# Performance work log

Measured on AMD Instinct MI355X. Metric: run time of the kernel, lower is better.

The kernel has to match this reference:

```python
import jax, jax.numpy as jnp
import numpy as np


def fps(pts, m):
    # pts: [N,3]; iterative farthest point sampling, deterministic start at index 0
    d0 = jnp.sum((pts - pts[0]) ** 2, axis=-1)  # [N]
    def step(mind, _):
        nxt = jnp.argmax(mind)
        d = jnp.sum((pts - pts[nxt]) ** 2, axis=-1)
        return jnp.minimum(mind, d), nxt
    _, idxs = jax.lax.scan(step, d0, None, length=m - 1)
    return jnp.concatenate([jnp.zeros((1,), idxs.dtype), idxs])  # [m]


def knn(queries, pts, k):
    # queries [M,3], pts [N,3] -> [M,k] indices of k nearest points (includes self)
    d = (jnp.sum(queries ** 2, -1, keepdims=True)
         - 2.0 * queries @ pts.T
         + jnp.sum(pts ** 2, -1)[None, :])  # [M,N]
    _, idx = jax.lax.top_k(-d, k)
    return idx


def mlp(x, params):
    # shared PointNet MLP: Linear+ReLU stack
    for w, b in params:
        x = jax.nn.relu(x @ w + b)
    return x


def sa_level(points, feats, ratio, k, params):
    # set-abstraction: fps downsample -> knn group -> shared MLP -> max pool per cluster
    B, N, _ = points.shape
    m = int(N * ratio)
    sel = jax.vmap(lambda p: fps(p, m))(points)                      # [B,m]
    npts = jnp.take_along_axis(points, sel[..., None], axis=1)       # [B,m,3]
    nbr = jax.vmap(knn, in_axes=(0, 0, None))(npts, points, k)       # [B,m,k]
    C = feats.shape[-1]
    kf = jnp.take_along_axis(feats, nbr.reshape(B, m * k, 1), axis=1).reshape(B, m, k, C)
    h = mlp(kf, params)                                              # [B,m,k,out]
    return npts, jnp.max(h, axis=2)                                  # [B,m,3], [B,m,out]


def setup_inputs() -> dict:
    key = jax.random.key(0)
    ks = jax.random.split(key, 20)
    points = jax.random.normal(ks[0], (8, 8192, 3), dtype=jnp.float32)
    batch = jnp.repeat(jnp.arange(8, dtype=jnp.int64), 8192)
    dims = {
        'pn1': [(3, 8), (8, 16), (16, 16)],
        'pn2': [(16, 32), (32, 64), (64, 64)],
        'pn3': [(64, 128), (128, 256), (256, 256)],
    }
    inp = {'points': points, 'batch': batch}
    i = 1
    for name, shapes in dims.items():
        for j, (cin, cout) in enumerate(shapes, start=1):
            inp[f'{name}_w{j}'] = jax.random.normal(ks[i], (cin, cout), dtype=jnp.float32) * (1.0 / np.sqrt(cin))
            inp[f'{name}_b{j}'] = jnp.zeros((cout,), dtype=jnp.float32)
            i += 1
    return inp


def reference(points, batch,
              pn1_w1, pn1_b1, pn1_w2, pn1_b2, pn1_w3, pn1_b3,
              pn2_w1, pn2_b1, pn2_w2, pn2_b2, pn2_w3, pn2_b3,
              pn3_w1, pn3_b1, pn3_w2, pn3_b2, pn3_w3, pn3_b3):
    # batch is implied by the uniform [B,N,3] layout (all clouds equal size)
    p1 = [(pn1_w1, pn1_b1), (pn1_w2, pn1_b2), (pn1_w3, pn1_b3)]
    p2 = [(pn2_w1, pn2_b1), (pn2_w2, pn2_b2), (pn2_w3, pn2_b3)]
    p3 = [(pn3_w1, pn3_b1), (pn3_w2, pn3_b2), (pn3_w3, pn3_b3)]
    pts1, f1 = sa_level(points, points, 0.25, 4, p1)   # [8,2048,3], [8,2048,16]
    pts2, f2 = sa_level(pts1, f1, 0.25, 4, p2)         # [8,512,3], [8,512,64]
    # level 3: cluster == batch -> global max pool per cloud
    out = jnp.max(mlp(f2, p3), axis=1)                  # [8,256]
    return out
```

## Files before the change

### kernel.cpp

```cpp
#include <hip/hip_runtime.h>
#include <stdint.h>

typedef unsigned long long u64;
typedef unsigned int u32;
typedef float f2 __attribute__((ext_vector_type(2)));

__device__ __forceinline__ float rn_mul(float a, float b){ return __fmul_rn(a,b); }
__device__ __forceinline__ float rn_add(float a, float b){ return __fadd_rn(a,b); }
__device__ __forceinline__ float rn_sub(float a, float b){ return __fsub_rn(a,b); }

__device__ __forceinline__ u32 fkey(float d){
  u32 b = __float_as_uint(d);
  return b ^ ((u32)((int)b >> 31) | 0x80000000u);
}

__device__ __forceinline__ u64 shfl_xor64(u64 v, int mask){
  int lo = __shfl_xor((int)(u32)v, mask, 64);
  int hi = __shfl_xor((int)(u32)(v >> 32), mask, 64);
  return ((u64)(u32)hi << 32) | (u32)lo;
}
__device__ __forceinline__ u64 umin64(u64 a, u64 b){ return a < b ? a : b; }
__device__ __forceinline__ u64 umax64(u64 a, u64 b){ return a > b ? a : b; }

template<int C>
__device__ __forceinline__ u64 dstep64(u64 v){
  const u32 l = (u32)__builtin_amdgcn_update_dpp((int)(u32)v, (int)(u32)v, C, 0xF, 0xF, false);
  const u32 h = (u32)__builtin_amdgcn_update_dpp((int)(u32)(v>>32), (int)(u32)(v>>32), C, 0xF, 0xF, false);
  const u64 o = ((u64)h << 32) | l;
  return o > v ? o : v;
}
__device__ __forceinline__ u64 wave64_max64(u64 v){
  v = dstep64<0x111>(v); v = dstep64<0x112>(v); v = dstep64<0x114>(v);
  v = dstep64<0x118>(v); v = dstep64<0x142>(v); v = dstep64<0x143>(v);
  return v;
}

template<int N, int NT, int M>
__global__ __launch_bounds__(NT)
void fps_kernel(const float* __restrict__ pts, float* __restrict__ npts)
{
#pragma clang fp contract(off)
  constexpr int PPT = N / NT;
  constexpr int PP2 = PPT / 2;
  constexpr int NW  = NT / 64;
  __shared__ float4 sp[N];
  __shared__ unsigned short WX[M];
  __shared__ u64 part[2][NW];
  const int b = blockIdx.x;
  const float* P = pts + (size_t)b * N * 3;
  float* O = npts + (size_t)b * M * 3;
  const int tid = threadIdx.x, lane = tid & 63, wv = tid >> 6;

  for (int i = tid; i < N; i += NT)
    sp[i] = make_float4(P[3*i+0], P[3*i+1], P[3*i+2], 0.0f);
  if (tid == 0) WX[0] = 0;
  __syncthreads();

  f2 rx[PP2], ry[PP2], rz[PP2], mind[PP2];
  const float4 c0 = sp[0];
  {
    const f2 cx2 = {c0.x,c0.x}, cy2 = {c0.y,c0.y}, cz2 = {c0.z,c0.z};
#pragma unroll
    for (int j = 0; j < PP2; ++j){
      const float4 va = sp[tid + (2*j+0)*NT];
      const float4 vb = sp[tid + (2*j+1)*NT];
      rx[j] = f2{va.x, vb.x}; ry[j] = f2{va.y, vb.y}; rz[j] = f2{va.z, vb.z};
      const f2 dx = rx[j]-cx2, dy = ry[j]-cy2, dz = rz[j]-cz2;
      mind[j] = ((dx*dx) + (dy*dy)) + (dz*dz);
    }
  }

#define LANEPK(dstpk)                                                         \
  {                                                                           \
    u64 p_[PPT];                                                              \
    _Pragma("unroll")                                                         \
    for (int k = 0; k < PPT; ++k){                                            \
      const float mk = (k&1) ? mind[k>>1].y : mind[k>>1].x;                   \
      p_[k] = ((u64)__float_as_uint(mk) << 32)                                \
            | (u64)(u32)~(u32)(tid + k*NT);                                   \
    }                                                                         \
    _Pragma("unroll")                                                         \
    for (int s = PPT/2; s > 0; s >>= 1)                                       \
      for (int i = 0; i < s; ++i) p_[i] = umax64(p_[i], p_[i+s]);             \
    (dstpk) = wave64_max64(p_[0]);                                            \
  }

  u64 mypk; LANEPK(mypk)

  for (int it = 1; it < M; ++it){
    if (lane == 63) part[it & 1][wv] = mypk;
    __syncthreads();
    u64 v = part[it & 1][lane & (NW-1)];
    v = dstep64<0x111>(v); v = dstep64<0x112>(v);
    const u32 wl = (u32)__builtin_amdgcn_readlane((int)(u32)v, 3);
    const u32 widx = ~wl;
    if (tid == 0) WX[it] = (unsigned short)widx;
    const float4 c = sp[widx];
    const f2 cx2 = {c.x,c.x}, cy2 = {c.y,c.y}, cz2 = {c.z,c.z};
#pragma unroll
    for (int j = 0; j < PP2; ++j){
      const f2 dx = rx[j]-cx2, dy = ry[j]-cy2, dz = rz[j]-cz2;
      const f2 d = ((dx*dx) + (dy*dy)) + (dz*dz);
      mind[j].x = fminf(mind[j].x, d.x);
      mind[j].y = fminf(mind[j].y, d.y);
    }
    LANEPK(mypk)
  }
  __syncthreads();
  for (int j = tid; j < M; j += NT){
    const float4 v = sp[WX[j]];
    O[3*j+0] = v.x; O[3*j+1] = v.y; O[3*j+2] = v.z;
  }
#undef LANEPK
}

__device__ __forceinline__ void top4_insert(u64& a0,u64& a1,u64& a2,u64& a3, u64 p){
  if (p < a3){
    const bool c2 = p < a2, c1 = p < a1, c0 = p < a0;
    const u64 n3 = c2 ? a2 : p;
    const u64 n2 = c2 ? (c1 ? a1 : p) : a2;
    const u64 n1 = c1 ? (c0 ? a0 : p) : a1;
    const u64 n0 = c0 ? p : a0;
    a0=n0; a1=n1; a2=n2; a3=n3;
  }
}

__device__ __forceinline__ void merge4_local(u64& a0,u64& a1,u64& a2,u64& a3,
                                             u64 b0,u64 b1,u64 b2,u64 b3){
  const u64 m0 = umin64(a0, b3);
  const u64 m1 = umin64(a1, b2);
  const u64 m2 = umin64(a2, b1);
  const u64 m3 = umin64(a3, b0);
  const u64 lo02 = umin64(m0,m2), hi02 = umax64(m0,m2);
  const u64 lo13 = umin64(m1,m3), hi13 = umax64(m1,m3);
  a0 = umin64(lo02, lo13); a1 = umax64(lo02, lo13);
  a2 = umin64(hi02, hi13); a3 = umax64(hi02, hi13);
}

__device__ __forceinline__ void merge4(u64& a0, u64& a1, u64& a2, u64& a3, int st)
{
  const u64 b0 = shfl_xor64(a0, st);
  const u64 b1 = shfl_xor64(a1, st);
  const u64 b2 = shfl_xor64(a2, st);
  const u64 b3 = shfl_xor64(a3, st);
  merge4_local(a0,a1,a2,a3, b0,b1,b2,b3);
}

template<int N, int M, int CH>
__global__ __launch_bounds__(256)
void knn_mlp1_kernel(const float* __restrict__ q, const float* __restrict__ pts,
                     const float* __restrict__ w1, const float* __restrict__ b1,
                     const float* __restrict__ w2, const float* __restrict__ b2,
                     const float* __restrict__ w3, const float* __restrict__ b3,
                     float* __restrict__ f1)
{
  __shared__ float4 s4[CH];
  constexpr int QPB = 64;
  const int blk = blockIdx.x;
  const int b = blk / (M / QPB);
  const int chunk = blk % (M / QPB);
  const int tid = threadIdx.x;
  const int g = tid >> 2;
  const int r = tid & 3;
  const int qi = chunk * QPB + g;
  const float* qp = q + ((size_t)b * M + qi) * 3;
  const float qx = qp[0], qy = qp[1], qz = qp[2];
  const float sumq = rn_add(rn_add(rn_mul(qx,qx), rn_mul(qy,qy)), rn_mul(qz,qz));
  const float* P = pts + (size_t)b * N * 3;

  u64 a0=~0ull, a1=~0ull, a2=~0ull, a3=~0ull;
  u64 e0=~0ull, e1=~0ull, e2=~0ull, e3=~0ull;
  for (int c0 = 0; c0 < N; c0 += CH){
    for (int i = tid; i < CH; i += 256){
      const float x = P[3*(c0+i)+0], y = P[3*(c0+i)+1], z = P[3*(c0+i)+2];
      s4[i] = make_float4(x, y, z,
          rn_add(rn_add(rn_mul(x,x), rn_mul(y,y)), rn_mul(z,z)));
    }
    __syncthreads();
#pragma unroll 2
    for (int jj = r; jj < CH; jj += 8){
      { const float4 v = s4[jj];
        const float dot = rn_add(rn_add(rn_mul(qx,v.x), rn_mul(qy,v.y)),
                                 rn_mul(qz,v.z));
        const float d = rn_add(rn_sub(sumq, rn_mul(2.0f, dot)), v.w);
        top4_insert(a0,a1,a2,a3, ((u64)fkey(d) << 32) | (u32)(c0+jj)); }
      { const float4 v = s4[jj+4];
        const float dot = rn_add(rn_add(rn_mul(qx,v.x), rn_mul(qy,v.y)),
                                 rn_mul(qz,v.z));
        const float d = rn_add(rn_sub(sumq, rn_mul(2.0f, dot)), v.w);
        top4_insert(e0,e1,e2,e3, ((u64)fkey(d) << 32) | (u32)(c0+jj+4)); }
    }
    __syncthreads();
  }
  merge4_local(a0,a1,a2,a3, e0,e1,e2,e3);
  merge4(a0,a1,a2,a3,1);
  merge4(a0,a1,a2,a3,2);
  const u64 selp = (r==0) ? a0 : (r==1) ? a1 : (r==2) ? a2 : a3;
  const u32 nidx = (u32)selp;

  const float nx = P[3*nidx+0], ny = P[3*nidx+1], nz = P[3*nidx+2];
  float h1[8];
#pragma unroll
  for (int c = 0; c < 8; ++c){
    float acc = b1[c];
    acc = fmaf(nx, w1[0*8+c], acc);
    acc = fmaf(ny, w1[1*8+c], acc);
    acc = fmaf(nz, w1[2*8+c], acc);
    h1[c] = fmaxf(acc, 0.0f);
  }
  float h2[16];
#pragma unroll
  for (int c = 0; c < 16; ++c){
    float acc = b2[c];
#pragma unroll
    for (int k = 0; k < 8; ++k) acc = fmaf(h1[k], w2[k*16+c], acc);
    h2[c] = fmaxf(acc, 0.0f);
  }
  float* fo = f1 + ((size_t)b * M + qi) * 16;
#pragma unroll
  for (int c = 0; c < 16; ++c){
    float acc = b3[c];
#pragma unroll
    for (int k = 0; k < 16; ++k) acc = fmaf(h2[k], w3[k*16+c], acc);
    float v = fmaxf(acc, 0.0f);
    v = fmaxf(v, __shfl_xor(v, 1, 64));
    v = fmaxf(v, __shfl_xor(v, 2, 64));
    if (r == 0) fo[c] = v;
  }
}

__global__ __launch_bounds__(256)
void knn_mlp2_kernel(const float* __restrict__ q, const float* __restrict__ pts,
                     const float* __restrict__ f1,
                     const float* __restrict__ w1, const float* __restrict__ b1,
                     const float* __restrict__ w2, const float* __restrict__ b2,
                     const float* __restrict__ w3, const float* __restrict__ b3,
                     float* __restrict__ f2)
{
  constexpr int N = 2048, M = 512, QPB = 64, QSTR = 2048;
  __shared__ float4 s4[N];
  const int blk = blockIdx.x;
  const int b = blk / (M / QPB);
  const int chunk = blk % (M / QPB);
  const int tid = threadIdx.x;
  const int g = tid >> 2;
  const int r = tid & 3;
  const int qi = chunk * QPB + g;
  const float* qp = q + ((size_t)b * QSTR + qi) * 3;
  const float qx = qp[0], qy = qp[1], qz = qp[2];
  const float sumq = rn_add(rn_add(rn_mul(qx,qx), rn_mul(qy,qy)), rn_mul(qz,qz));
  const float* P = pts + (size_t)b * N * 3;

  for (int i = tid; i < N; i += 256){
    const float x = P[3*i+0], y = P[3*i+1], z = P[3*i+2];
    s4[i] = make_float4(x, y, z,
        rn_add(rn_add(rn_mul(x,x), rn_mul(y,y)), rn_mul(z,z)));
  }
  __syncthreads();

  u64 a0=~0ull, a1=~0ull, a2=~0ull, a3=~0ull;
  u64 e0=~0ull, e1=~0ull, e2=~0ull, e3=~0ull;
#pragma unroll 2
  for (int j = r; j < N; j += 8){
    { const float4 v = s4[j];
      const float dot = rn_add(rn_add(rn_mul(qx,v.x), rn_mul(qy,v.y)),
                               rn_mul(qz,v.z));
      const float d = rn_add(rn_sub(sumq, rn_mul(2.0f, dot)), v.w);
      top4_insert(a0,a1,a2,a3, ((u64)fkey(d) << 32) | (u32)j); }
    { const float4 v = s4[j+4];
      const float dot = rn_add(rn_add(rn_mul(qx,v.x), rn_mul(qy,v.y)),
                               rn_mul(qz,v.z));
      const float d = rn_add(rn_sub(sumq, rn_mul(2.0f, dot)), v.w);
      top4_insert(e0,e1,e2,e3, ((u64)fkey(d) << 32) | (u32)(j+4)); }
  }
  merge4_local(a0,a1,a2,a3, e0,e1,e2,e3);
  merge4(a0,a1,a2,a3,1);
  merge4(a0,a1,a2,a3,2);
  const u64 selp = (r==0) ? a0 : (r==1) ? a1 : (r==2) ? a2 : a3;
  const u32 nidx = (u32)selp;

  const float* fv = f1 + ((size_t)b * 2048 + nidx) * 16;
  float x[16];
#pragma unroll
  for (int i = 0; i < 4; ++i){
    const float4 v = ((const float4*)fv)[i];
    x[4*i+0]=v.x; x[4*i+1]=v.y; x[4*i+2]=v.z; x[4*i+3]=v.w;
  }
  float h1[32];
#pragma unroll
  for (int c = 0; c < 32; ++c){
    float acc = b1[c];
#pragma unroll
    for (int k = 0; k < 16; ++k) acc = fmaf(x[k], w1[k*32+c], acc);
    h1[c] = fmaxf(acc, 0.0f);
  }
  float h2[64];
#pragma unroll
  for (int c = 0; c < 64; ++c){
    float acc = b2[c];
#pragma unroll
    for (int k = 0; k < 32; ++k) acc = fmaf(h1[k], w2[k*64+c], acc);
    h2[c] = fmaxf(acc, 0.0f);
  }
  float* fo = f2 + ((size_t)b * M + qi) * 64;
#pragma unroll
  for (int c = 0; c < 64; ++c){
    float acc = b3[c];
#pragma unroll
    for (int k = 0; k < 64; ++k) acc = fmaf(h2[k], w3[k*64+c], acc);
    float v = fmaxf(acc, 0.0f);
    v = fmaxf(v, __shfl_xor(v, 1, 64));
    v = fmaxf(v, __shfl_xor(v, 2, 64));
    if (r == 0) fo[c] = v;
  }
}

__global__ __launch_bounds__(256)
void mlp3_kernel(const float* __restrict__ f2,
                 const float* __restrict__ w1, const float* __restrict__ b1,
                 const float* __restrict__ w2, const float* __restrict__ b2,
                 const float* __restrict__ w3, const float* __restrict__ b3,
                 float* __restrict__ out)
{
  constexpr int P = 16;
  __shared__ float X [P][64];
  __shared__ float H1[P][128];
  __shared__ float H2[P][256];
  __shared__ float PM[4][256];
  const int blk = blockIdx.x;
  const int b  = blk >> 5;
  const int pc = blk & 31;
  const int tid = threadIdx.x;
  const float* F = f2 + ((size_t)b * 512 + (size_t)pc * P) * 64;
  { const float4 v = ((const float4*)F)[tid]; ((float4*)&X[0][0])[tid] = v; }
  __syncthreads();
  {
    const int p = tid >> 4, c0 = (tid & 15) * 8;
    float acc[8];
#pragma unroll
    for (int i = 0; i < 8; ++i) acc[i] = b1[c0+i];
    for (int k = 0; k < 64; ++k){
      const float xv = X[p][k];
      const float4 wa = *(const float4*)&w1[k*128 + c0];
      const float4 wb = *(const float4*)&w1[k*128 + c0 + 4];
      acc[0]=fmaf(xv,wa.x,acc[0]); acc[1]=fmaf(xv,wa.y,acc[1]);
      acc[2]=fmaf(xv,wa.z,acc[2]); acc[3]=fmaf(xv,wa.w,acc[3]);
      acc[4]=fmaf(xv,wb.x,acc[4]); acc[5]=fmaf(xv,wb.y,acc[5]);
      acc[6]=fmaf(xv,wb.z,acc[6]); acc[7]=fmaf(xv,wb.w,acc[7]);
    }
#pragma unroll
    for (int i = 0; i < 8; ++i) H1[p][c0+i] = fmaxf(acc[i], 0.0f);
  }
  __syncthreads();
  {
    const int p = tid >> 4, c0 = (tid & 15) * 16;
    float acc[16];
#pragma unroll
    for (int i = 0; i < 16; ++i) acc[i] = b2[c0+i];
    for (int k = 0; k < 128; ++k){
      const float xv = H1[p][k];
#pragma unroll
      for (int i4 = 0; i4 < 4; ++i4){
        const float4 wv = *(const float4*)&w2[k*256 + c0 + 4*i4];
        acc[4*i4+0]=fmaf(xv,wv.x,acc[4*i4+0]);
        acc[4*i4+1]=fmaf(xv,wv.y,acc[4*i4+1]);
        acc[4*i4+2]=fmaf(xv,wv.z,acc[4*i4+2]);
        acc[4*i4+3]=fmaf(xv,wv.w,acc[4*i4+3]);
      }
    }
#pragma unroll
    for (int i = 0; i < 16; ++i) H2[p][c0+i] = fmaxf(acc[i], 0.0f);
  }
  __syncthreads();
  {
    const int pg = tid >> 6, c0 = (tid & 63) * 4;
    float acc[4][4];
#pragma unroll
    for (int p4 = 0; p4 < 4; ++p4)
#pragma unroll
      for (int i = 0; i < 4; ++i) acc[p4][i] = b3[c0+i];
    for (int k = 0; k < 256; ++k){
      const float4 wv = *(const float4*)&w3[k*256 + c0];
#pragma unroll
      for (int p4 = 0; p4 < 4; ++p4){
        const float xv = H2[pg*4+p4][k];
        acc[p4][0]=fmaf(xv,wv.x,acc[p4][0]);
        acc[p4][1]=fmaf(xv,wv.y,acc[p4][1]);
        acc[p4][2]=fmaf(xv,wv.z,acc[p4][2]);
        acc[p4][3]=fmaf(xv,wv.w,acc[p4][3]);
      }
    }
    float4 mx;
    mx.x = fmaxf(fmaxf(fmaxf(acc[0][0],0.f),fmaxf(acc[1][0],0.f)),
                 fmaxf(fmaxf(acc[2][0],0.f),fmaxf(acc[3][0],0.f)));
    mx.y = fmaxf(fmaxf(fmaxf(acc[0][1],0.f),fmaxf(acc[1][1],0.f)),
                 fmaxf(fmaxf(acc[2][1],0.f),fmaxf(acc[3][1],0.f)));
    mx.z = fmaxf(fmaxf(fmaxf(acc[0][2],0.f),fmaxf(acc[1][2],0.f)),
                 fmaxf(fmaxf(acc[2][2],0.f),fmaxf(acc[3][2],0.f)));
    mx.w = fmaxf(fmaxf(fmaxf(acc[0][3],0.f),fmaxf(acc[1][3],0.f)),
                 fmaxf(fmaxf(acc[2][3],0.f),fmaxf(acc[3][3],0.f)));
    *(float4*)&PM[pg][c0] = mx;
  }
  __syncthreads();
  {
    const float m = fmaxf(fmaxf(PM[0][tid], PM[1][tid]),
                          fmaxf(PM[2][tid], PM[3][tid]));
    atomicMax((int*)(out + b*256 + tid), __float_as_int(m));
  }
}

extern "C" void kernel_launch(void* const* d_in, const int* in_sizes, int n_in,
                              void* d_out, int out_size, void* d_ws, size_t ws_size,
                              hipStream_t stream)
{
  const float* pts  = (const float*)d_in[0];
  const float* p1w1 = (const float*)d_in[2];
  const float* p1b1 = (const float*)d_in[3];
  const float* p1w2 = (const float*)d_in[4];
  const float* p1b2 = (const float*)d_in[5];
  const float* p1w3 = (const float*)d_in[6];
  const float* p1b3 = (const float*)d_in[7];
  const float* p2w1 = (const float*)d_in[8];
  const float* p2b1 = (const float*)d_in[9];
  const float* p2w2 = (const float*)d_in[10];
  const float* p2b2 = (const float*)d_in[11];
  const float* p2w3 = (const float*)d_in[12];
  const float* p2b3 = (const float*)d_in[13];
  const float* p3w1 = (const float*)d_in[14];
  const float* p3b1 = (const float*)d_in[15];
  const float* p3w2 = (const float*)d_in[16];
  const float* p3b2 = (const float*)d_in[17];
  const float* p3w3 = (const float*)d_in[18];
  const float* p3b3 = (const float*)d_in[19];

  float* ws = (float*)d_ws;
  size_t o = 0;
  float* npts1 = ws + o; o += (size_t)8*2048*3;
  float* f1    = ws + o; o += (size_t)8*2048*16;
  float* f2    = ws + o; o += (size_t)8*512*64;

  fps_kernel<8192,256,2048><<<8, 256, 0, stream>>>(pts, npts1);
  knn_mlp1_kernel<8192,2048,2048><<<8*32, 256, 0, stream>>>(npts1, pts,
      p1w1, p1b1, p1w2, p1b2, p1w3, p1b3, f1);
  knn_mlp2_kernel<<<8*8, 256, 0, stream>>>(npts1, npts1, f1,
      p2w1, p2b1, p2w2, p2b2, p2w3, p2b3, f2);
  hipMemsetAsync(d_out, 0, (size_t)out_size * sizeof(float), stream);
  mlp3_kernel<<<8*32, 256, 0, stream>>>(f2,
      p3w1, p3b1, p3w2, p3b2, p3w3, p3b3, (float*)d_out);
}
```

Measured before the change: 2.268 ms.

## Speculatively select two FPS points per iteration using top-2 candidates

Each FPS round now extracts the top-2 candidates per thread, wave and block. When the runner-up is at least as far from the winner as its own current min distance, it is provably the next argmax, so two points are committed in one round. This halves the number of block-wide barriers and reductions on the serial critical path when the test passes. The cost is a heavier top-2 reduction each round, a branch, and subtle tie-break correctness concerns. The block size also doubles to 512 threads to spread the per-point distance work.

```diff
diff --git a/kernel.cpp b/kernel.cpp
--- a/kernel.cpp
+++ b/kernel.cpp
@@ -33,6 +33,14 @@
   v = dstep64<0x111>(v); v = dstep64<0x112>(v); v = dstep64<0x114>(v);
   v = dstep64<0x118>(v); v = dstep64<0x142>(v); v = dstep64<0x143>(v);
   return v;
+}
+__device__ __forceinline__ u64 readlane64(u64 v, int l){
+  const u32 lo = (u32)__builtin_amdgcn_readlane((int)(u32)v, l);
+  const u32 hi = (u32)__builtin_amdgcn_readlane((int)(u32)(v>>32), l);
+  return ((u64)hi << 32) | lo;
+}
+__device__ __forceinline__ f2 f2max(f2 a, f2 b){
+  f2 r; r.x = fmaxf(a.x,b.x); r.y = fmaxf(a.y,b.y); return r;
 }
 
 template<int N, int NT, int M>
@@ -45,11 +53,12 @@
   constexpr int NW  = NT / 64;
   __shared__ float4 sp[N];
   __shared__ unsigned short WX[M];
-  __shared__ u64 part[2][NW];
+  __shared__ u64 part[2][NW][2];
   const int b = blockIdx.x;
   const float* P = pts + (size_t)b * N * 3;
   float* O = npts + (size_t)b * M * 3;
   const int tid = threadIdx.x, lane = tid & 63, wv = tid >> 6;
+  const float NEGINF = __uint_as_float(0xff800000u);
 
   for (int i = tid; i < N; i += NT)
     sp[i] = make_float4(P[3*i+0], P[3*i+1], P[3*i+2], 0.0f);
@@ -70,48 +79,95 @@
     }
   }
 
-#define LANEPK(dstpk)                                                         \
+#define VALK(k) (((k)&1) ? mind[(k)>>1].y : mind[(k)>>1].x)
+
+#define EXTRACT_PUBLISH(slot)                                                 \
   {                                                                           \
-    u64 p_[PPT];                                                              \
+    f2 t[PP2];                                                                \
     _Pragma("unroll")                                                         \
-    for (int k = 0; k < PPT; ++k){                                            \
-      const float mk = (k&1) ? mind[k>>1].y : mind[k>>1].x;                   \
-      p_[k] = ((u64)__float_as_uint(mk) << 32)                                \
-            | (u64)(u32)~(u32)(tid + k*NT);                                   \
-    }                                                                         \
+    for (int j = 0; j < PP2; ++j) t[j] = mind[j];                             \
     _Pragma("unroll")                                                         \
-    for (int s = PPT/2; s > 0; s >>= 1)                                       \
-      for (int i = 0; i < s; ++i) p_[i] = umax64(p_[i], p_[i+s]);             \
-    (dstpk) = wave64_max64(p_[0]);                                            \
-  }
-
-  u64 mypk; LANEPK(mypk)
-
-  for (int it = 1; it < M; ++it){
-    if (lane == 63) part[it & 1][wv] = mypk;
+    for (int s = PP2/2; s > 0; s >>= 1)                                       \
+      for (int i = 0; i < s; ++i) t[i] = f2max(t[i], t[i+s]);                 \
+    const float bm = fmaxf(t[0].x, t[0].y);                                   \
+    int k1 = 0;                                                               \
+    _Pragma("unroll")                                                         \
+    for (int k = PPT-1; k >= 0; --k) if (VALK(k) == bm) k1 = k;               \
+    float bm2 = NEGINF;                                                       \
+    _Pragma("unroll")                                                         \
+    for (int k = 0; k < PPT; ++k)                                             \
+      bm2 = fmaxf(bm2, (k == k1) ? NEGINF : VALK(k));                         \
+    int k2 = 0;                                                               \
+    _Pragma("unroll")                                                         \
+    for (int k = PPT-1; k >= 0; --k)                                          \
+      if (k != k1 && VALK(k) == bm2) k2 = k;                                  \
+    const u64 p1 = ((u64)__float_as_uint(bm)  << 32)                          \
+                 | (u64)(u32)~(u32)(tid + k1*NT);                             \
+    const u64 p2 = ((u64)__float_as_uint(bm2) << 32)                          \
+                 | (u64)(u32)~(u32)(tid + k2*NT);                             \
+    const u64 w1 = readlane64(wave64_max64(p1), 63);                          \
+    const u64 cand = (p1 == w1) ? p2 : p1;                                    \
+    const u64 w2 = readlane64(wave64_max64(cand), 63);                        \
+    if (lane == 63){ part[slot][wv][0] = w1; part[slot][wv][1] = w2; }        \
+  }
+
+  EXTRACT_PUBLISH(1)
+
+  int it = 1, rc = 1;
+  while (it < M){
     __syncthreads();
-    u64 v = part[it & 1][lane & (NW-1)];
-    v = dstep64<0x111>(v); v = dstep64<0x112>(v);
-    const u32 wl = (u32)__builtin_amdgcn_readlane((int)(u32)v, 3);
-    const u32 widx = ~wl;
-    if (tid == 0) WX[it] = (unsigned short)widx;
-    const float4 c = sp[widx];
-    const f2 cx2 = {c.x,c.x}, cy2 = {c.y,c.y}, cz2 = {c.z,c.z};
-#pragma unroll
-    for (int j = 0; j < PP2; ++j){
-      const f2 dx = rx[j]-cx2, dy = ry[j]-cy2, dz = rz[j]-cz2;
-      const f2 d = ((dx*dx) + (dy*dy)) + (dz*dz);
-      mind[j].x = fminf(mind[j].x, d.x);
-      mind[j].y = fminf(mind[j].y, d.y);
-    }
-    LANEPK(mypk)
+    const int p = rc & 1;
+    const u64 a  = part[p][lane & (NW-1)][0];
+    const u64 bq = part[p][lane & (NW-1)][1];
+    u64 v = a;
+    v = dstep64<0x111>(v); v = dstep64<0x112>(v); v = dstep64<0x114>(v);
+    const u64 g1 = readlane64(v, 7);
+    u64 c_ = (a == g1) ? bq : a;
+    c_ = dstep64<0x111>(c_); c_ = dstep64<0x112>(c_); c_ = dstep64<0x114>(c_);
+    const u64 g2 = readlane64(c_, 7);
+    const u32 widx1 = ~(u32)g1;
+    const u32 widx2 = ~(u32)g2;
+    const float4 c1 = sp[widx1];
+    const float4 c2 = sp[widx2];
+    const float m2f = __uint_as_float((u32)(g2 >> 32));
+    const float dvx = c2.x - c1.x, dvy = c2.y - c1.y, dvz = c2.z - c1.z;
+    const float dv = ((dvx*dvx) + (dvy*dvy)) + (dvz*dvz);
+    const bool take2 = (dv >= m2f) && (it + 1 < M);
+    if (tid == 0){ WX[it] = (unsigned short)widx1;
+                   if (take2) WX[it+1] = (unsigned short)widx2; }
+    if (take2){
+      const f2 ax={c1.x,c1.x}, ay={c1.y,c1.y}, az={c1.z,c1.z};
+      const f2 bx={c2.x,c2.x}, by={c2.y,c2.y}, bz={c2.z,c2.z};
+#pragma unroll
+      for (int j = 0; j < PP2; ++j){
+        const f2 dx1 = rx[j]-ax, dy1 = ry[j]-ay, dz1 = rz[j]-az;
+        const f2 d1 = ((dx1*dx1) + (dy1*dy1)) + (dz1*dz1);
+        const f2 dx2 = rx[j]-bx, dy2 = ry[j]-by, dz2 = rz[j]-bz;
+        const f2 d2 = ((dx2*dx2) + (dy2*dy2)) + (dz2*dz2);
+        mind[j].x = fminf(fminf(mind[j].x, d1.x), d2.x);
+        mind[j].y = fminf(fminf(mind[j].y, d1.y), d2.y);
+      }
+    } else {
+      const f2 ax={c1.x,c1.x}, ay={c1.y,c1.y}, az={c1.z,c1.z};
+#pragma unroll
+      for (int j = 0; j < PP2; ++j){
+        const f2 dx1 = rx[j]-ax, dy1 = ry[j]-ay, dz1 = rz[j]-az;
+        const f2 d1 = ((dx1*dx1) + (dy1*dy1)) + (dz1*dz1);
+        mind[j].x = fminf(mind[j].x, d1.x);
+        mind[j].y = fminf(mind[j].y, d1.y);
+      }
+    }
+    EXTRACT_PUBLISH((rc+1) & 1)
+    it += take2 ? 2 : 1;
+    rc += 1;
   }
   __syncthreads();
   for (int j = tid; j < M; j += NT){
     const float4 v = sp[WX[j]];
     O[3*j+0] = v.x; O[3*j+1] = v.y; O[3*j+2] = v.z;
   }
-#undef LANEPK
+#undef EXTRACT_PUBLISH
+#undef VALK
 }
 
 __device__ __forceinline__ void top4_insert(u64& a0,u64& a1,u64& a2,u64& a3, u64 p){
@@ -439,7 +495,7 @@
   float* f1    = ws + o; o += (size_t)8*2048*16;
   float* f2    = ws + o; o += (size_t)8*512*64;
 
-  fps_kernel<8192,256,2048><<<8, 256, 0, stream>>>(pts, npts1);
+  fps_kernel<8192,512,2048><<<8, 512, 0, stream>>>(pts, npts1);
   knn_mlp1_kernel<8192,2048,2048><<<8*32, 256, 0, stream>>>(npts1, pts,
       p1w1, p1b1, p1w2, p1b2, p1w3, p1b3, f1);
   knn_mlp2_kernel<<<8*8, 256, 0, stream>>>(npts1, npts1, f1,
```

New measurement: 2.407 ms. 1.06x slower.
